# Kernel tuning notes

Measured on AMD Instinct MI355X. Metric: run time of the kernel, lower is better.

## Reference

```python
import jax, jax.numpy as jnp
import numpy as np

B, C, H, W = 8, 384, 32, 32
NH = 6
HD = C // NH          # 64
T = H * W             # 1024
EPS = 1e-5            # torch InstanceNorm2d default


def setup_inputs() -> dict:
    key = jax.random.key(0)
    ks = jax.random.split(key, 8)
    s = 1.0 / np.sqrt(C)  # keep pre-softmax logits in a sane range
    x = jax.random.normal(ks[0], (B, C, H, W), dtype=jnp.float32)
    Wq = jax.random.normal(ks[1], (C, C), dtype=jnp.float32) * s
    Wk = jax.random.normal(ks[2], (C, C), dtype=jnp.float32) * s
    Wv = jax.random.normal(ks[3], (C, C), dtype=jnp.float32) * s
    head_w = jax.random.normal(ks[4], (NH, NH), dtype=jnp.float32) * (1.0 / np.sqrt(NH))
    gamma = jnp.ones((NH,), dtype=jnp.float32)
    beta = jnp.zeros((NH,), dtype=jnp.float32)
    projW = jax.random.normal(ks[5], (C, C), dtype=jnp.float32) * s
    projb = jnp.zeros((C,), dtype=jnp.float32)
    return {"x": x, "Wq": Wq, "Wk": Wk, "Wv": Wv, "head_w": head_w,
            "gamma": gamma, "beta": beta, "projW": projW, "projb": projb}


def reference(x, Wq, Wk, Wv, head_w, gamma, beta, projW, projb):
    b, c, h, w = x.shape
    t = h * w
    scale = HD ** (-0.5)
    xf = x.reshape(b, c, t)                               # [B,C,T]
    # 1x1 convs == channel GEMMs; conv weight [Cout,Cin]
    q = jnp.einsum('oc,bct->bot', Wq, xf).reshape(b, NH, HD, t)
    k = jnp.einsum('oc,bct->bot', Wk, xf).reshape(b, NH, HD, t)
    v = jnp.einsum('oc,bct->bot', Wv, xf).reshape(b, NH, HD, t)
    # raw scores [B,h,T,T], scaled
    scores = jnp.einsum('bhdq,bhdt->bhqt', q, k) * scale
    # cross-head 1x1 conv mix: out-head g from in-head h
    mixed = jnp.einsum('gh,bhqt->bgqt', head_w, scores)
    attn = jax.nn.softmax(mixed, axis=-1)
    # InstanceNorm2d over spatial dims (q,T) per (b,head), biased variance
    mean = jnp.mean(attn, axis=(2, 3), keepdims=True)
    var = jnp.var(attn, axis=(2, 3), keepdims=True)
    attn = (attn - mean) * jax.lax.rsqrt(var + EPS)
    attn = attn * gamma[None, :, None, None] + beta[None, :, None, None]
    # value matmul: v is [B,h,d,T]
    out = jnp.einsum('bhqt,bhdt->bhqd', attn, v)          # [B,h,T,d]
    # faithful row-major reshape (matches torch .view(B, T, C))
    out = out.reshape(b, t, c)
    y = out @ projW.T + projb                              # Linear(C,C)
    return jnp.transpose(y, (0, 2, 1)).reshape(b, c, h, w)
```

## Files before the change

### kernel.cpp

```cpp
#include <hip/hip_runtime.h>
#include <hip/hip_bf16.h>
#include <cstdint>

typedef __bf16 bf16_t;
typedef __bf16 bf16x8 __attribute__((ext_vector_type(8)));
typedef float  f32x4  __attribute__((ext_vector_type(4)));
typedef int    i32x4  __attribute__((ext_vector_type(4)));

#define MFMA16(a, b, c) __builtin_amdgcn_mfma_f32_16x16x32_bf16((a), (b), (c), 0, 0, 0)

constexpr int BB = 8, CC = 384, NHH = 6, TT = 1024;

union U8 { uint4 u; bf16_t h[8]; };
union U2 { unsigned int u; bf16_t h[2]; };
union I4B { i32x4 i; bf16x8 v; };

static __device__ __forceinline__ void gload_lds16(const void* g, void* l) {
    __builtin_amdgcn_global_load_lds((const __attribute__((address_space(1))) void*)g,
                                     (__attribute__((address_space(3))) void*)l, 16, 0, 0);
}

static __device__ __forceinline__ bf16x8 cvt8(const float* p) {
    f32x4 a = *(const f32x4*)p, b = *(const f32x4*)(p + 4);
    U8 o;
    #pragma unroll
    for (int j = 0; j < 4; ++j) { o.h[j] = (bf16_t)a[j]; o.h[4 + j] = (bf16_t)b[j]; }
    return *(bf16x8*)&o;
}

__global__ __launch_bounds__(256) void qkv_kernel(
    const float* __restrict__ x,
    const float* __restrict__ Wq,
    const float* __restrict__ Wk,
    const float* __restrict__ Wv,
    bf16_t* __restrict__ qT,
    bf16_t* __restrict__ kT,
    bf16_t* __restrict__ vm,
    float*  __restrict__ vrs)
{
    const int og = blockIdx.x;
    const int tt = blockIdx.y;
    const int b  = blockIdx.z;
    const int t0 = tt * 64;
    const int tid  = threadIdx.x;
    const int lane = tid & 63;
    const int wid  = tid >> 6;
    const int quad = lane >> 4;
    const int l16  = lane & 15;

    __shared__ __align__(16) bf16_t xT[64][CC + 8];

    {
        const float* xb = x + (size_t)b * CC * TT;
        const int tq = tid & 7;
        const int cp = tid >> 3;
        #pragma unroll
        for (int pass = 0; pass < 6; ++pass) {
            const int c = (pass * 32 + cp) * 2;
            const float* r0 = xb + (size_t)c * TT + t0 + tq * 8;
            const float* r1 = r0 + TT;
            f32x4 a0 = *(const f32x4*)r0, a1 = *(const f32x4*)(r0 + 4);
            f32x4 b0 = *(const f32x4*)r1, b1 = *(const f32x4*)(r1 + 4);
            #pragma unroll
            for (int j = 0; j < 8; ++j) {
                U2 p;
                p.h[0] = (bf16_t)((j < 4) ? a0[j] : a1[j - 4]);
                p.h[1] = (bf16_t)((j < 4) ? b0[j] : b1[j - 4]);
                *(unsigned int*)&xT[tq * 8 + j][c] = p.u;
            }
        }
    }
    __syncthreads();

    const float* W = (og < 2) ? Wq : (og < 4) ? Wk : Wv;
    const int obase = (og & 1) * 192 + wid * 48;

    if (og < 4) {
        f32x4 acc[3][4];
        const f32x4 zero = {0.f, 0.f, 0.f, 0.f};
        #pragma unroll
        for (int mi = 0; mi < 3; ++mi)
            #pragma unroll
            for (int ni = 0; ni < 4; ++ni) acc[mi][ni] = zero;

        for (int k0 = 0; k0 < CC; k0 += 32) {
            bf16x8 afr[3];
            #pragma unroll
            for (int mi = 0; mi < 3; ++mi)
                afr[mi] = cvt8(W + (size_t)(obase + mi * 16 + l16) * CC + k0 + quad * 8);
            #pragma unroll
            for (int ni = 0; ni < 4; ++ni) {
                bf16x8 bfr = *(const bf16x8*)&xT[ni * 16 + l16][k0 + quad * 8];
                #pragma unroll
                for (int mi = 0; mi < 3; ++mi)
                    acc[mi][ni] = MFMA16(afr[mi], bfr, acc[mi][ni]);
            }
        }

        bf16_t* dst = (og < 2) ? qT : kT;
        #pragma unroll
        for (int mi = 0; mi < 3; ++mi)
            #pragma unroll
            for (int ni = 0; ni < 4; ++ni) {
                const int o0 = obase + mi * 16 + quad * 4;
                const int tl = t0 + ni * 16 + l16;
                U2 lo2, hi2;
                lo2.h[0] = (bf16_t)acc[mi][ni][0]; lo2.h[1] = (bf16_t)acc[mi][ni][1];
                hi2.h[0] = (bf16_t)acc[mi][ni][2]; hi2.h[1] = (bf16_t)acc[mi][ni][3];
                uint2 pk; pk.x = lo2.u; pk.y = hi2.u;
                *(uint2*)(dst + ((size_t)b * TT + tl) * CC + o0) = pk;
            }
    } else {
        f32x4 acc[4][3];
        const f32x4 zero = {0.f, 0.f, 0.f, 0.f};
        #pragma unroll
        for (int mi = 0; mi < 4; ++mi)
            #pragma unroll
            for (int ni = 0; ni < 3; ++ni) acc[mi][ni] = zero;

        for (int k0 = 0; k0 < CC; k0 += 32) {
            bf16x8 bfr[3];
            #pragma unroll
            for (int ni = 0; ni < 3; ++ni)
                bfr[ni] = cvt8(W + (size_t)(obase + ni * 16 + l16) * CC + k0 + quad * 8);
            #pragma unroll
            for (int mi = 0; mi < 4; ++mi) {
                bf16x8 afr = *(const bf16x8*)&xT[mi * 16 + l16][k0 + quad * 8];
                #pragma unroll
                for (int ni = 0; ni < 3; ++ni)
                    acc[mi][ni] = MFMA16(afr, bfr[ni], acc[mi][ni]);
            }
        }

        #pragma unroll
        for (int mi = 0; mi < 4; ++mi)
            #pragma unroll
            for (int ni = 0; ni < 3; ++ni) {
                const int ol  = obase + ni * 16 + l16;
                const int tl0 = mi * 16 + quad * 4;
                U2 lo2, hi2;
                lo2.h[0] = (bf16_t)acc[mi][ni][0]; lo2.h[1] = (bf16_t)acc[mi][ni][1];
                hi2.h[0] = (bf16_t)acc[mi][ni][2]; hi2.h[1] = (bf16_t)acc[mi][ni][3];
                uint2 pk; pk.x = lo2.u; pk.y = hi2.u;
                *(uint2*)(vm + ((size_t)b * CC + ol) * TT + t0 + tl0) = pk;
            }

        #pragma unroll
        for (int ni = 0; ni < 3; ++ni) {
            float s = 0.f;
            #pragma unroll
            for (int mi = 0; mi < 4; ++mi)
                #pragma unroll
                for (int r = 0; r < 4; ++r) s += acc[mi][ni][r];
            s += __shfl_xor(s, 16, 64);
            s += __shfl_xor(s, 32, 64);
            if (quad == 0)
                atomicAdd(&vrs[b * CC + obase + ni * 16 + l16], s);
        }
    }
}

__global__ __launch_bounds__(256, 1) void fused_attn(
    const bf16_t* __restrict__ qT,
    const bf16_t* __restrict__ kT,
    const bf16_t* __restrict__ vm,
    const float*  __restrict__ head_w,
    float* __restrict__ Uhat,
    float* __restrict__ sq)
{
    const int L  = blockIdx.x;
    const int b  = L & 7;
    const int qt = L >> 3;

    const int tid = threadIdx.x, lane = tid & 63, wid = tid >> 6;
    const int quad = lane >> 4, l16 = lane & 15;
    const int qg = wid & 1, ts = wid >> 1;

    __shared__ __align__(16) bf16_t sm[49152];
    bf16_t* Ks = sm;

    float mixc[36];
    #pragma unroll
    for (int j = 0; j < 36; ++j) {
        const float v = 0.125f * head_w[j];
        mixc[j] = __uint_as_float(__builtin_amdgcn_readfirstlane(__float_as_uint(v)));
    }

    bf16x8 qf[6][2];
    {
        const bf16_t* qp = qT + ((size_t)b * TT + qt * 32 + qg * 16 + l16) * CC + quad * 8;
        #pragma unroll
        for (int h = 0; h < 6; ++h)
            #pragma unroll
            for (int k2 = 0; k2 < 2; ++k2)
                qf[h][k2] = *(const bf16x8*)(qp + h * 64 + k2 * 32);
    }

    int koff[12], voff[12];
    #pragma unroll
    for (int i = 0; i < 12; ++i) {
        const int f = i * 256 + tid;
        const int krow = f / 48, kc = f - krow * 48;
        koff[i] = krow * CC + ((kc & 56) | ((kc ^ krow) & 7)) * 8;
        const int vrow = f >> 3, vc = f & 7;
        voff[i] = vrow * TT + ((vc ^ (vrow & 7)) * 8);
    }
    const bf16_t* kTb = kT + (size_t)b * TT * CC;
    const bf16_t* vmb = vm + (size_t)b * CC * TT;
    char* KsB = (char*)sm;
    char* VsB = (char*)sm + 49152;
    const int ldst = tid * 16;

    #pragma unroll
    for (int i = 0; i < 12; ++i)
        gload_lds16(kTb + koff[i], KsB + i * 4096 + ldst);

    f32x4 U[6][4];
    const f32x4 zero = {0.f, 0.f, 0.f, 0.f};
    #pragma unroll
    for (int h = 0; h < 6; ++h)
        #pragma unroll
        for (int d = 0; d < 4; ++d) U[h][d] = zero;
    float lacc[6]  = {0.f, 0.f, 0.f, 0.f, 0.f, 0.f};
    float l2acc[6] = {0.f, 0.f, 0.f, 0.f, 0.f, 0.f};

    const int  s3    = l16 & 7;
    const int  rbase = ts * 32;
    const int  addrA = ((quad & 1) * 32 + l16) * 4;
    const int  addrB = addrA + 64;
    const bool qlo   = (quad < 2);

    __syncthreads();

    for (int tt = 0; tt < 16; ++tt) {
        #pragma unroll
        for (int i = 0; i < 12; ++i)
            gload_lds16(vmb + tt * 64 + voff[i], VsB + i * 4096 + ldst);

        f32x4 S[6][2];
        #pragma unroll
        for (int h = 0; h < 6; ++h) {
            #pragma unroll
            for (int blk = 0; blk < 2; ++blk) {
                const bf16_t* Ar = Ks + (size_t)(rbase + blk * 16 + l16) * CC + h * 64;
                bf16x8 a0 = *(const bf16x8*)(Ar + ((quad ^ s3) * 8));
                bf16x8 a1 = *(const bf16x8*)(Ar + (((4 + quad) ^ s3) * 8));
                f32x4 s = MFMA16(a0, qf[h][0], zero);
                S[h][blk] = MFMA16(a1, qf[h][1], s);
            }
        }

        bf16x8 pa[6];
        #pragma unroll
        for (int g = 0; g < 6; ++g) {
            unsigned int uu[2][2];
            #pragma unroll
            for (int blk = 0; blk < 2; ++blk) {
                f32x4 m = mixc[g * 6] * S[0][blk];
                #pragma unroll
                for (int h2 = 1; h2 < 6; ++h2) m += mixc[g * 6 + h2] * S[h2][blk];
                f32x4 pv;
                #pragma unroll
                for (int r = 0; r < 4; ++r) pv[r] = __expf(fminf(m[r], 60.0f));
                lacc[g]  += pv[0] + pv[1] + pv[2] + pv[3];
                l2acc[g] += pv[0] * pv[0] + pv[1] * pv[1] + pv[2] * pv[2] + pv[3] * pv[3];
                U2 lo, hi;
                lo.h[0] = (bf16_t)pv[0]; lo.h[1] = (bf16_t)pv[1];
                hi.h[0] = (bf16_t)pv[2]; hi.h[1] = (bf16_t)pv[3];
                uu[blk][0] = lo.u; uu[blk][1] = hi.u;
            }
            int x0 = __builtin_amdgcn_ds_bpermute(addrA, (int)uu[0][0]);
            int y0 = __builtin_amdgcn_ds_bpermute(addrA, (int)uu[1][0]);
            int x1 = __builtin_amdgcn_ds_bpermute(addrA, (int)uu[0][1]);
            int y1 = __builtin_amdgcn_ds_bpermute(addrA, (int)uu[1][1]);
            int x2 = __builtin_amdgcn_ds_bpermute(addrB, (int)uu[0][0]);
            int y2 = __builtin_amdgcn_ds_bpermute(addrB, (int)uu[1][0]);
            int x3 = __builtin_amdgcn_ds_bpermute(addrB, (int)uu[0][1]);
            int y3 = __builtin_amdgcn_ds_bpermute(addrB, (int)uu[1][1]);
            I4B c;
            c.i = (i32x4){qlo ? x0 : y0, qlo ? x1 : y1, qlo ? x2 : y2, qlo ? x3 : y3};
            pa[g] = c.v;
        }

        __syncthreads();

        if (tt < 15) {
            #pragma unroll
            for (int i = 0; i < 12; ++i)
                gload_lds16(kTb + (size_t)(tt + 1) * 64 * CC + koff[i], KsB + i * 4096 + ldst);
        }

        const bf16_t* Vb = sm + 24576;
        #pragma unroll
        for (int h = 0; h < 6; ++h) {
            #pragma unroll
            for (int n2 = 0; n2 < 4; ++n2) {
                bf16x8 bv = *(const bf16x8*)(Vb + (size_t)(h * 64 + n2 * 16 + l16) * 64
                                             + (((ts * 4 + quad) ^ s3) * 8));
                U[h][n2] = MFMA16(pa[h], bv, U[h][n2]);
            }
        }

        __syncthreads();
    }

    float* MB   = (float*)sm;
    float* Lh   = MB + 12288;
    float* L2h  = Lh + 192;
    float* lnvT = L2h + 192;

    float lrow[6], l2row[6];
    #pragma unroll
    for (int g = 0; g < 6; ++g) {
        float l = lacc[g], l2 = l2acc[g];
        l  += __shfl_xor(l, 16, 64);  l  += __shfl_xor(l, 32, 64);
        l2 += __shfl_xor(l2, 16, 64); l2 += __shfl_xor(l2, 32, 64);
        lrow[g] = l; l2row[g] = l2;
    }

    if (ts == 1) {
        #pragma unroll
        for (int h = 0; h < 6; ++h)
            #pragma unroll
            for (int n2 = 0; n2 < 4; ++n2)
                #pragma unroll
                for (int r = 0; r < 4; ++r)
                    MB[(size_t)((qg * 6 + h) * 16 + quad * 4 + r) * 64 + n2 * 16 + l16] = U[h][n2][r];
        if (quad == 0) {
            #pragma unroll
            for (int g = 0; g < 6; ++g) {
                Lh [(qg * 6 + g) * 16 + l16] = lrow[g];
                L2h[(qg * 6 + g) * 16 + l16] = l2row[g];
            }
        }
    }
    __syncthreads();

    if (ts == 0) {
        float linvq[6];
        #pragma unroll
        for (int g = 0; g < 6; ++g) {
            lrow[g]  += Lh [(qg * 6 + g) * 16 + l16];
            l2row[g] += L2h[(qg * 6 + g) * 16 + l16];
            linvq[g] = 1.0f / lrow[g];
        }
        #pragma unroll
        for (int g = 0; g < 6; ++g) {
            float c = l2row[g] * linvq[g] * linvq[g];
            c += __shfl_xor(c, 1, 64); c += __shfl_xor(c, 2, 64);
            c += __shfl_xor(c, 4, 64); c += __shfl_xor(c, 8, 64);
            if (lane == 0) atomicAdd(&sq[b * NHH + g], c);
        }
        if (quad == 0) {
            #pragma unroll
            for (int g = 0; g < 6; ++g)
                lnvT[(qg * 6 + g) * 16 + l16] = linvq[g];
        }
        #pragma unroll
        for (int h = 0; h < 6; ++h) {
            float* Ub = Uhat + ((size_t)(b * NHH + h) * TT + qt * 32 + qg * 16) * 64;
            #pragma unroll
            for (int n2 = 0; n2 < 4; ++n2)
                #pragma unroll
                for (int r = 0; r < 4; ++r) {
                    const float u = U[h][n2][r]
                        + MB[(size_t)((qg * 6 + h) * 16 + quad * 4 + r) * 64 + n2 * 16 + l16];
                    const float li = lnvT[(qg * 6 + h) * 16 + quad * 4 + r];
                    __builtin_nontemporal_store(u * li,
                        Ub + (size_t)(quad * 4 + r) * 64 + n2 * 16 + l16);
                }
        }
    }
}

__global__ __launch_bounds__(256) void proj_kernel(
    const float* __restrict__ Uhat,
    const float* __restrict__ vrs,
    const float* __restrict__ sumsq,
    const float* __restrict__ gamma,
    const float* __restrict__ beta,
    const float* __restrict__ projW,
    const float* __restrict__ projb,
    float* __restrict__ out)
{
    const int ts = blockIdx.x;
    const int b  = blockIdx.y;
    const int t0 = ts * 32;
    const int tid = threadIdx.x, lane = tid & 63, wid = tid >> 6;
    const int quad = lane >> 4, l16 = lane & 15;

    __shared__ float Ac[6], Cc[6], pb[CC];
    if (tid < 6) {
        const float ss  = sumsq[b * NHH + tid];
        const float var = fmaxf(ss - 1.0f, 0.0f) * (1.0f / 1048576.0f);
        const float a   = gamma[tid] * rsqrtf(var + 1e-5f);
        Ac[tid] = a;
        Cc[tid] = beta[tid] - a * (1.0f / 1024.0f);
    }
    for (int i = tid; i < CC; i += 256) pb[i] = projb[i];
    __syncthreads();

    f32x4 acc[6][2];
    const f32x4 zero = {0.f, 0.f, 0.f, 0.f};
    #pragma unroll
    for (int mi = 0; mi < 6; ++mi)
        #pragma unroll
        for (int ni = 0; ni < 2; ++ni) acc[mi][ni] = zero;

    const float* Ub = Uhat + (size_t)b * TT * CC;
    for (int k0 = 0; k0 < CC; k0 += 32) {
        bf16x8 bfr[2];
        #pragma unroll
        for (int ni = 0; ni < 2; ++ni) {
            const int tl = t0 + ni * 16 + l16;
            const int baseoff = tl * CC + k0 + quad * 8;
            const int hh = baseoff >> 16;
            const float A  = Ac[hh];
            const float Cb = Cc[hh];
            f32x4 u0 = __builtin_nontemporal_load((const f32x4*)(Ub + baseoff));
            f32x4 u1 = __builtin_nontemporal_load((const f32x4*)(Ub + baseoff + 4));
            U8 z;
            #pragma unroll
            for (int j = 0; j < 8; ++j) {
                const int d = (baseoff + j) & 63;
                const float uv = (j < 4) ? u0[j] : u1[j - 4];
                z.h[j] = (bf16_t)(A * uv + Cb * vrs[b * CC + hh * 64 + d]);
            }
            bfr[ni] = *(const bf16x8*)&z;
        }
        #pragma unroll
        for (int mi = 0; mi < 6; ++mi) {
            const int o = wid * 96 + mi * 16 + l16;
            bf16x8 afr = cvt8(projW + (size_t)o * CC + k0 + quad * 8);
            #pragma unroll
            for (int ni = 0; ni < 2; ++ni)
                acc[mi][ni] = MFMA16(afr, bfr[ni], acc[mi][ni]);
        }
    }

    #pragma unroll
    for (int mi = 0; mi < 6; ++mi)
        #pragma unroll
        for (int ni = 0; ni < 2; ++ni)
            #pragma unroll
            for (int r = 0; r < 4; ++r) {
                const int o  = wid * 96 + mi * 16 + quad * 4 + r;
                const int tl = t0 + ni * 16 + l16;
                out[((size_t)b * CC + o) * TT + tl] = acc[mi][ni][r] + pb[o];
            }
}

extern "C" void kernel_launch(void* const* d_in, const int* in_sizes, int n_in,
                              void* d_out, int out_size, void* d_ws, size_t ws_size,
                              hipStream_t stream)
{
    float* outp = (float*)d_out;
    char* ws = (char*)d_ws;

    size_t off = 0;
    auto alloc = [&](size_t bytes) {
        void* p = ws + off;
        off += (bytes + 255) & ~(size_t)255;
        return p;
    };

    const size_t szT = (size_t)BB * TT * CC * sizeof(bf16_t);

    bf16_t* qTb = (bf16_t*)alloc(szT);
    bf16_t* kTb = (bf16_t*)alloc(szT);
    bf16_t* vmb = (bf16_t*)alloc(szT);
    float*  Uh  = (float*)alloc((size_t)BB * NHH * TT * 64 * sizeof(float));
    float*  vr  = (float*)alloc((size_t)BB * CC * sizeof(float));
    float*  sq  = (float*)alloc(48 * sizeof(float));

    hipMemsetAsync(vr, 0, (size_t)BB * CC * sizeof(float), stream);
    hipMemsetAsync(sq, 0, 48 * sizeof(float), stream);
    qkv_kernel<<<dim3(6, 16, 8), 256, 0, stream>>>(
        (const float*)d_in[0], (const float*)d_in[1], (const float*)d_in[2],
        (const float*)d_in[3], qTb, kTb, vmb, vr);
    fused_attn<<<256, 256, 0, stream>>>(
        qTb, kTb, vmb, (const float*)d_in[4], Uh, sq);
    proj_kernel<<<dim3(32, 8), 256, 0, stream>>>(
        Uh, vr, sq, (const float*)d_in[5], (const float*)d_in[6],
        (const float*)d_in[7], (const float*)d_in[8], outp);
}
```

Baseline: 246.4 us.

## Split attention key range across two blocks and add stats reduction kernel

The attention kernel now uses 512-thread blocks covering 64 query rows and only half the keys (split-K). Each block writes unnormalized partial U and row-sum partials, and a new stats kernel combines them into 1/l and the variance sums. The projection kernel then adds the two partials, applies the normalization, and switches to 16-token tiles for more blocks. The point is better occupancy and parallelism in attention, paid for with doubled U traffic and an extra kernel launch.

```diff
diff --git a/kernel.cpp b/kernel.cpp
--- a/kernel.cpp
+++ b/kernel.cpp
@@ -38,8 +38,8 @@
     bf16_t* __restrict__ vm,
     float*  __restrict__ vrs)
 {
-    const int og = blockIdx.x;
-    const int tt = blockIdx.y;
+    const int tt = blockIdx.x;
+    const int og = blockIdx.y;
     const int b  = blockIdx.z;
     const int t0 = tt * 64;
     const int tid  = threadIdx.x;
@@ -160,24 +160,28 @@
     }
 }
 
-__global__ __launch_bounds__(256, 1) void fused_attn(
+__global__ __launch_bounds__(512, 2) void fused_attn(
     const bf16_t* __restrict__ qT,
     const bf16_t* __restrict__ kT,
     const bf16_t* __restrict__ vm,
     const float*  __restrict__ head_w,
-    float* __restrict__ Uhat,
-    float* __restrict__ sq)
+    float* __restrict__ Up,
+    float* __restrict__ lp,
+    float* __restrict__ l2p)
 {
     const int L  = blockIdx.x;
     const int b  = L & 7;
-    const int qt = L >> 3;
+    const int rr = L >> 3;
+    const int qt = rr & 15;
+    const int th = rr >> 4;
 
     const int tid = threadIdx.x, lane = tid & 63, wid = tid >> 6;
     const int quad = lane >> 4, l16 = lane & 15;
-    const int qg = wid & 1, ts = wid >> 1;
+    const int qg = wid & 3, ts = wid >> 2;
 
     __shared__ __align__(16) bf16_t sm[49152];
     bf16_t* Ks = sm;
+    __shared__ float Lh[384], L2h[384];
 
     float mixc[36];
     #pragma unroll
@@ -188,7 +192,7 @@
 
     bf16x8 qf[6][2];
     {
-        const bf16_t* qp = qT + ((size_t)b * TT + qt * 32 + qg * 16 + l16) * CC + quad * 8;
+        const bf16_t* qp = qT + ((size_t)b * TT + qt * 64 + qg * 16 + l16) * CC + quad * 8;
         #pragma unroll
         for (int h = 0; h < 6; ++h)
             #pragma unroll
@@ -196,24 +200,24 @@
                 qf[h][k2] = *(const bf16x8*)(qp + h * 64 + k2 * 32);
     }
 
-    int koff[12], voff[12];
-    #pragma unroll
-    for (int i = 0; i < 12; ++i) {
-        const int f = i * 256 + tid;
+    int koff[6], voff[6];
+    #pragma unroll
+    for (int i = 0; i < 6; ++i) {
+        const int f = i * 512 + tid;
         const int krow = f / 48, kc = f - krow * 48;
         koff[i] = krow * CC + ((kc & 56) | ((kc ^ krow) & 7)) * 8;
         const int vrow = f >> 3, vc = f & 7;
         voff[i] = vrow * TT + ((vc ^ (vrow & 7)) * 8);
     }
-    const bf16_t* kTb = kT + (size_t)b * TT * CC;
-    const bf16_t* vmb = vm + (size_t)b * CC * TT;
+    const bf16_t* kTb = kT + ((size_t)b * TT + th * 512) * CC;
+    const bf16_t* vmb = vm + (size_t)b * CC * TT + th * 512;
     char* KsB = (char*)sm;
     char* VsB = (char*)sm + 49152;
     const int ldst = tid * 16;
 
     #pragma unroll
-    for (int i = 0; i < 12; ++i)
-        gload_lds16(kTb + koff[i], KsB + i * 4096 + ldst);
+    for (int i = 0; i < 6; ++i)
+        gload_lds16(kTb + koff[i], KsB + i * 8192 + ldst);
 
     f32x4 U[6][4];
     const f32x4 zero = {0.f, 0.f, 0.f, 0.f};
@@ -232,10 +236,10 @@
 
     __syncthreads();
 
-    for (int tt = 0; tt < 16; ++tt) {
-        #pragma unroll
-        for (int i = 0; i < 12; ++i)
-            gload_lds16(vmb + tt * 64 + voff[i], VsB + i * 4096 + ldst);
+    for (int tt = 0; tt < 8; ++tt) {
+        #pragma unroll
+        for (int i = 0; i < 6; ++i)
+            gload_lds16(vmb + tt * 64 + voff[i], VsB + i * 8192 + ldst);
 
         f32x4 S[6][2];
         #pragma unroll
@@ -284,10 +288,10 @@
 
         __syncthreads();
 
-        if (tt < 15) {
-            #pragma unroll
-            for (int i = 0; i < 12; ++i)
-                gload_lds16(kTb + (size_t)(tt + 1) * 64 * CC + koff[i], KsB + i * 4096 + ldst);
+        if (tt < 7) {
+            #pragma unroll
+            for (int i = 0; i < 6; ++i)
+                gload_lds16(kTb + (size_t)(tt + 1) * 64 * CC + koff[i], KsB + i * 8192 + ldst);
         }
 
         const bf16_t* Vb = sm + 24576;
@@ -304,10 +308,7 @@
         __syncthreads();
     }
 
-    float* MB   = (float*)sm;
-    float* Lh   = MB + 12288;
-    float* L2h  = Lh + 192;
-    float* lnvT = L2h + 192;
+    float* MB = (float*)sm;
 
     float lrow[6], l2row[6];
     #pragma unroll
@@ -337,44 +338,54 @@
     __syncthreads();
 
     if (ts == 0) {
-        float linvq[6];
-        #pragma unroll
-        for (int g = 0; g < 6; ++g) {
-            lrow[g]  += Lh [(qg * 6 + g) * 16 + l16];
-            l2row[g] += L2h[(qg * 6 + g) * 16 + l16];
-            linvq[g] = 1.0f / lrow[g];
-        }
-        #pragma unroll
-        for (int g = 0; g < 6; ++g) {
-            float c = l2row[g] * linvq[g] * linvq[g];
-            c += __shfl_xor(c, 1, 64); c += __shfl_xor(c, 2, 64);
-            c += __shfl_xor(c, 4, 64); c += __shfl_xor(c, 8, 64);
-            if (lane == 0) atomicAdd(&sq[b * NHH + g], c);
-        }
         if (quad == 0) {
             #pragma unroll
-            for (int g = 0; g < 6; ++g)
-                lnvT[(qg * 6 + g) * 16 + l16] = linvq[g];
+            for (int g = 0; g < 6; ++g) {
+                const size_t o = ((size_t)th * 48 + b * 6 + g) * TT + qt * 64 + qg * 16 + l16;
+                lp[o]  = lrow[g]  + Lh [(qg * 6 + g) * 16 + l16];
+                l2p[o] = l2row[g] + L2h[(qg * 6 + g) * 16 + l16];
+            }
         }
         #pragma unroll
         for (int h = 0; h < 6; ++h) {
-            float* Ub = Uhat + ((size_t)(b * NHH + h) * TT + qt * 32 + qg * 16) * 64;
+            float* Ub = Up + ((((size_t)th * 8 + b) * 6 + h) * TT + qt * 64 + qg * 16) * 64;
             #pragma unroll
             for (int n2 = 0; n2 < 4; ++n2)
                 #pragma unroll
                 for (int r = 0; r < 4; ++r) {
                     const float u = U[h][n2][r]
                         + MB[(size_t)((qg * 6 + h) * 16 + quad * 4 + r) * 64 + n2 * 16 + l16];
-                    const float li = lnvT[(qg * 6 + h) * 16 + quad * 4 + r];
-                    __builtin_nontemporal_store(u * li,
+                    __builtin_nontemporal_store(u,
                         Ub + (size_t)(quad * 4 + r) * 64 + n2 * 16 + l16);
                 }
         }
     }
 }
 
+__global__ __launch_bounds__(256) void stats_kernel(
+    const float* __restrict__ lp, const float* __restrict__ l2p,
+    float* __restrict__ linv, float* __restrict__ sq)
+{
+    const int bg = blockIdx.x, tid = threadIdx.x;
+    float c = 0.f;
+    for (int q = tid; q < TT; q += 256) {
+        const float l  = lp [(size_t)bg * TT + q] + lp [(size_t)(48 + bg) * TT + q];
+        const float l2 = l2p[(size_t)bg * TT + q] + l2p[(size_t)(48 + bg) * TT + q];
+        const float inv = 1.0f / l;
+        linv[bg * TT + q] = inv;
+        c += l2 * inv * inv;
+    }
+    #pragma unroll
+    for (int off = 1; off < 64; off <<= 1) c += __shfl_xor(c, off, 64);
+    __shared__ float red[4];
+    if ((tid & 63) == 0) red[tid >> 6] = c;
+    __syncthreads();
+    if (tid == 0) sq[bg] = red[0] + red[1] + red[2] + red[3];
+}
+
 __global__ __launch_bounds__(256) void proj_kernel(
-    const float* __restrict__ Uhat,
+    const float* __restrict__ Up,
+    const float* __restrict__ linv,
     const float* __restrict__ vrs,
     const float* __restrict__ sumsq,
     const float* __restrict__ gamma,
@@ -385,7 +396,7 @@
 {
     const int ts = blockIdx.x;
     const int b  = blockIdx.y;
-    const int t0 = ts * 32;
+    const int t0 = ts * 16;
     const int tid = threadIdx.x, lane = tid & 63, wid = tid >> 6;
     const int quad = lane >> 4, l16 = lane & 15;
 
@@ -400,54 +411,49 @@
     for (int i = tid; i < CC; i += 256) pb[i] = projb[i];
     __syncthreads();
 
-    f32x4 acc[6][2];
+    f32x4 acc[6];
     const f32x4 zero = {0.f, 0.f, 0.f, 0.f};
     #pragma unroll
-    for (int mi = 0; mi < 6; ++mi)
-        #pragma unroll
-        for (int ni = 0; ni < 2; ++ni) acc[mi][ni] = zero;
-
-    const float* Ub = Uhat + (size_t)b * TT * CC;
+    for (int mi = 0; mi < 6; ++mi) acc[mi] = zero;
+
+    constexpr size_t PST = (size_t)BB * NHH * TT * 64;
+    const float* U0 = Up + (size_t)b * (NHH * TT * 64);
+    const float* U1 = U0 + PST;
     for (int k0 = 0; k0 < CC; k0 += 32) {
-        bf16x8 bfr[2];
-        #pragma unroll
-        for (int ni = 0; ni < 2; ++ni) {
-            const int tl = t0 + ni * 16 + l16;
-            const int baseoff = tl * CC + k0 + quad * 8;
-            const int hh = baseoff >> 16;
-            const float A  = Ac[hh];
-            const float Cb = Cc[hh];
-            f32x4 u0 = __builtin_nontemporal_load((const f32x4*)(Ub + baseoff));
-            f32x4 u1 = __builtin_nontemporal_load((const f32x4*)(Ub + baseoff + 4));
-            U8 z;
-            #pragma unroll
-            for (int j = 0; j < 8; ++j) {
-                const int d = (baseoff + j) & 63;
-                const float uv = (j < 4) ? u0[j] : u1[j - 4];
-                z.h[j] = (bf16_t)(A * uv + Cb * vrs[b * CC + hh * 64 + d]);
-            }
-            bfr[ni] = *(const bf16x8*)&z;
-        }
+        const int tl = t0 + l16;
+        const int baseoff = tl * CC + k0 + quad * 8;
+        const int hh = baseoff >> 16;
+        const int d0 = baseoff & 63;
+        const float li = linv[b * 6144 + (baseoff >> 6)];
+        const float Al = Ac[hh] * li;
+        const float Cb = Cc[hh];
+        f32x4 u0 = __builtin_nontemporal_load((const f32x4*)(U0 + baseoff))
+                 + __builtin_nontemporal_load((const f32x4*)(U1 + baseoff));
+        f32x4 u1 = __builtin_nontemporal_load((const f32x4*)(U0 + baseoff + 4))
+                 + __builtin_nontemporal_load((const f32x4*)(U1 + baseoff + 4));
+        U8 z;
+        #pragma unroll
+        for (int j = 0; j < 8; ++j) {
+            const float uv = (j < 4) ? u0[j] : u1[j - 4];
+            z.h[j] = (bf16_t)(Al * uv + Cb * vrs[b * CC + hh * 64 + d0 + j]);
+        }
+        bf16x8 bfr = *(const bf16x8*)&z;
         #pragma unroll
         for (int mi = 0; mi < 6; ++mi) {
             const int o = wid * 96 + mi * 16 + l16;
             bf16x8 afr = cvt8(projW + (size_t)o * CC + k0 + quad * 8);
-            #pragma unroll
-            for (int ni = 0; ni < 2; ++ni)
-                acc[mi][ni] = MFMA16(afr, bfr[ni], acc[mi][ni]);
+            acc[mi] = MFMA16(afr, bfr, acc[mi]);
         }
     }
 
     #pragma unroll
     for (int mi = 0; mi < 6; ++mi)
         #pragma unroll
-        for (int ni = 0; ni < 2; ++ni)
-            #pragma unroll
-            for (int r = 0; r < 4; ++r) {
-                const int o  = wid * 96 + mi * 16 + quad * 4 + r;
-                const int tl = t0 + ni * 16 + l16;
-                out[((size_t)b * CC + o) * TT + tl] = acc[mi][ni][r] + pb[o];
-            }
+        for (int r = 0; r < 4; ++r) {
+            const int o  = wid * 96 + mi * 16 + quad * 4 + r;
+            const int tl = t0 + l16;
+            out[((size_t)b * CC + o) * TT + tl] = acc[mi][r] + pb[o];
+        }
 }
 
 extern "C" void kernel_launch(void* const* d_in, const int* in_sizes, int n_in,
@@ -469,18 +475,21 @@
     bf16_t* qTb = (bf16_t*)alloc(szT);
     bf16_t* kTb = (bf16_t*)alloc(szT);
     bf16_t* vmb = (bf16_t*)alloc(szT);
-    float*  Uh  = (float*)alloc((size_t)BB * NHH * TT * 64 * sizeof(float));
+    float*  Uh  = (float*)alloc((size_t)2 * BB * NHH * TT * 64 * sizeof(float));
+    float*  lpb = (float*)alloc((size_t)2 * 48 * TT * sizeof(float));
+    float*  l2b = (float*)alloc((size_t)2 * 48 * TT * sizeof(float));
+    float*  lv  = (float*)alloc((size_t)48 * TT * sizeof(float));
     float*  vr  = (float*)alloc((size_t)BB * CC * sizeof(float));
     float*  sq  = (float*)alloc(48 * sizeof(float));
 
     hipMemsetAsync(vr, 0, (size_t)BB * CC * sizeof(float), stream);
-    hipMemsetAsync(sq, 0, 48 * sizeof(float), stream);
-    qkv_kernel<<<dim3(6, 16, 8), 256, 0, stream>>>(
+    qkv_kernel<<<dim3(16, 6, 8), 256, 0, stream>>>(
         (const float*)d_in[0], (const float*)d_in[1], (const float*)d_in[2],
         (const float*)d_in[3], qTb, kTb, vmb, vr);
-    fused_attn<<<256, 256, 0, stream>>>(
-        qTb, kTb, vmb, (const float*)d_in[4], Uh, sq);
-    proj_kernel<<<dim3(32, 8), 256, 0, stream>>>(
-        Uh, vr, sq, (const float*)d_in[5], (const float*)d_in[6],
+    fused_attn<<<256, 512, 0, stream>>>(
+        qTb, kTb, vmb, (const float*)d_in[4], Uh, lpb, l2b);
+    stats_kernel<<<48, 256, 0, stream>>>(lpb, l2b, lv, sq);
+    proj_kernel<<<dim3(64, 8), 256, 0, stream>>>(
+        Uh, lv, vr, sq, (const float*)d_in[5], (const float*)d_in[6],
         (const float*)d_in[7], (const float*)d_in[8], outp);
 }
```

New measurement: 352.5 us. 1.43x slower.
